# Performance work log

Measured on AMD Instinct MI355X. Metric: run time of the kernel, lower is better.

Reference implementation:

```python
import jax, jax.numpy as jnp
import numpy as np

N_CLIN = 38
N_PIX = 36
N_NODES = N_CLIN + N_PIX  # 74
FV = 128
B = 1024
HID = 512
N_OUT = 1


def _base_edges():
    # Faithful to Network.get_edges: self-edges for all nodes, then for each
    # pixel node i, bidirectional edges to every clinical node.
    ids = np.arange(N_NODES)
    parts = [np.stack([ids, ids])]
    c = np.arange(N_CLIN)
    for i in range(N_CLIN, N_NODES):
        ii = np.full(N_CLIN, i)
        parts.append(np.stack([ii, c]))
        parts.append(np.stack([c, ii]))
    return np.concatenate(parts, axis=1)  # (2, 2810)


def setup_inputs() -> dict:
    key = jax.random.key(0)
    ks = jax.random.split(key, 10)
    base = _base_edges()  # (2, E0)
    # Batched edge index: per-sample copy offset by ind*N_NODES (batch-major order,
    # matching the torch.cat loop).
    offs = np.arange(B)[None, :, None] * N_NODES  # (1, B, 1)
    edge_index = (base[:, None, :] + offs).reshape(2, -1)  # (2, B*E0)
    s = 1.0 / np.sqrt(FV)
    return {
        "clinical_embeddings": jax.random.normal(ks[0], (B, N_CLIN, FV), jnp.float32),
        "image_embeddings": jax.random.normal(ks[1], (B, N_PIX, FV), jnp.float32),
        # RMRM graph-net params (single message-passing layer, fv_dim -> fv_dim)
        "W_self": jax.random.normal(ks[2], (FV, FV), jnp.float32) * s,
        "W_msg": jax.random.normal(ks[3], (FV, FV), jnp.float32) * s,
        "b_g": jnp.zeros((FV,), jnp.float32),
        # OutputBlock MLP params: fv_dim*(n_clinical+1)=4992 -> 512 -> 1
        "W1": jax.random.normal(ks[4], (FV * (N_CLIN + 1), HID), jnp.float32) * (1.0 / np.sqrt(FV * (N_CLIN + 1))),
        "b1": jnp.zeros((HID,), jnp.float32),
        "W2": jax.random.normal(ks[5], (HID, N_OUT), jnp.float32) * (1.0 / np.sqrt(HID)),
        "b2": jnp.zeros((N_OUT,), jnp.float32),
        "edge_index": jnp.asarray(edge_index, jnp.int32),
    }


def reference(clinical_embeddings, image_embeddings, W_self, W_msg, b_g, W1, b1, W2, b2, edge_index):
    # Assemble node features: [B, n_nodes, fv] -> flat [B*n_nodes, fv]
    x = jnp.concatenate([clinical_embeddings, image_embeddings], axis=1)
    x = x.reshape(-1, FV)
    src, dst = edge_index[0], edge_index[1]
    n_total = B * N_NODES
    # Mean-aggregated message passing (RMRM layer): gather + segment-sum
    msg = jax.ops.segment_sum(x[src], dst, num_segments=n_total)  # [B*N, FV]
    deg = jax.ops.segment_sum(jnp.ones_like(src, jnp.float32), dst, num_segments=n_total)
    agg = msg / deg[:, None]
    h = jax.nn.relu(x @ W_self + agg @ W_msg + b_g)  # [B*N, FV]
    h = h.reshape(B, N_NODES, FV)
    graph_fvs_c = h[:, :N_CLIN]          # [B, 38, FV]
    graph_fvs_i = h[:, N_CLIN:]          # [B, 36, FV]
    # AvgPool2d(6,6) over [B, FV, 6, 6] == mean over the 36 pixel nodes
    gap = graph_fvs_i.mean(axis=1)       # [B, FV]
    combined = jnp.concatenate([graph_fvs_c, gap[:, None, :]], axis=1).reshape(B, -1)
    # OutputBlock MLP
    out = jax.nn.relu(combined @ W1 + b1) @ W2 + b2  # [B, 1]
    return out
```

## Files before the change

### kernel.cpp

```cpp
#include <hip/hip_runtime.h>

#define FV 128
#define NCLIN 38
#define NPIX 36
#define NTOT 74
#define BATCH 1024
#define HID 512
#define COMB 4992
#define XPAD 136

typedef __attribute__((ext_vector_type(4))) float f32x4;
typedef __attribute__((ext_vector_type(8))) short s16x8;

#define WS_WCT  0
#define WS_WIT  8192
#define WS_WMT  16384
#define WS_COMB 24576
#define WS_W1T  2580480
#define WS_Z    3858432
#define ZSTRIDE (BATCH * HID)

__device__ __forceinline__ unsigned short bf16_rne(float f) {
    union { float f; unsigned int u; } v; v.f = f;
    unsigned int u = v.u;
    u += 0x7fffu + ((u >> 16) & 1u);
    return (unsigned short)(u >> 16);
}
__device__ __forceinline__ float bf2f(unsigned short h) {
    union { unsigned int u; float f; } v; v.u = ((unsigned int)h) << 16;
    return v.f;
}

__global__ __launch_bounds__(256) void k_static(
    const float* __restrict__ W1, const float* __restrict__ wself,
    const float* __restrict__ wmsg, float* __restrict__ ws)
{
    const int t = threadIdx.x;
    if (blockIdx.x == 78) {
        unsigned short* WcT = (unsigned short*)(ws + WS_WCT);
        unsigned short* WiT = (unsigned short*)(ws + WS_WIT);
        unsigned short* WmT = (unsigned short*)(ws + WS_WMT);
        const int r  = blockIdx.y * 16 + (t >> 4);
        const int f0 = (t & 15) * 8;
#pragma unroll
        for (int j = 0; j < 8; ++j) {
            const int f = f0 + j;
            const int idx = r * 128 + f;
            const float wm = wmsg[idx];
            const float s  = wself[idx];
            WcT[f * 128 + r] = bf16_rne(s + wm * (1.0f / 37.0f));
            WiT[f * 128 + r] = bf16_rne(s + wm * (1.0f / 39.0f));
            WmT[f * 128 + r] = bf16_rne(wm);
        }
        return;
    }
    unsigned short* W1T = (unsigned short*)(ws + WS_W1T);
    const int k0 = blockIdx.x * 64;
    const int n0 = blockIdx.y * 64;
    __shared__ float tile[64][65];
    const int r16 = t >> 4;
    const int c4  = (t & 15) * 4;
#pragma unroll
    for (int p = 0; p < 4; ++p) {
        const int r = p * 16 + r16;
        const float4 v = *(const float4*)&W1[(size_t)(k0 + r) * HID + n0 + c4];
        tile[r][c4 + 0] = v.x; tile[r][c4 + 1] = v.y;
        tile[r][c4 + 2] = v.z; tile[r][c4 + 3] = v.w;
    }
    __syncthreads();
    const int j  = t >> 2;
    const int i0 = (t & 3) * 16;
    unsigned short tmp[16];
#pragma unroll
    for (int s = 0; s < 16; ++s) tmp[s] = bf16_rne(tile[i0 + s][j]);
    unsigned short* dst = &W1T[(size_t)(n0 + j) * COMB + k0 + i0];
    *(uint4*)&dst[0] = *(uint4*)&tmp[0];
    *(uint4*)&dst[8] = *(uint4*)&tmp[8];
}

__global__ __launch_bounds__(256) void k_batch(
    const float* __restrict__ clin, const float* __restrict__ img,
    const float* __restrict__ bg, float* __restrict__ ws)
{
    const int b = blockIdx.x;
    const int t = threadIdx.x;

    __shared__ __align__(16) unsigned short xl[NTOT * XPAD];
    __shared__ __align__(16) unsigned short sab[2 * 128];
    __shared__ float tcv[128];
    __shared__ float tiv[128];

    const float* xc = clin + (size_t)b * NCLIN * FV;
    const float* xi = img  + (size_t)b * NPIX * FV;
    for (int i = t; i < NCLIN * 32; i += 256) {
        const int row = i >> 5, c4 = (i & 31) * 4;
        const float4 v = *(const float4*)&xc[row * 128 + c4];
        ushort4 u;
        u.x = bf16_rne(v.x); u.y = bf16_rne(v.y);
        u.z = bf16_rne(v.z); u.w = bf16_rne(v.w);
        *(ushort4*)&xl[row * XPAD + c4] = u;
    }
    for (int i = t; i < NPIX * 32; i += 256) {
        const int row = i >> 5, c4 = (i & 31) * 4;
        const float4 v = *(const float4*)&xi[row * 128 + c4];
        ushort4 u;
        u.x = bf16_rne(v.x); u.y = bf16_rne(v.y);
        u.z = bf16_rne(v.z); u.w = bf16_rne(v.w);
        *(ushort4*)&xl[(NCLIN + row) * XPAD + c4] = u;
    }
    __syncthreads();

    const int f = t & 127;
    if (t < 128) {
        float s = 0.f;
#pragma unroll
        for (int n = 0; n < NCLIN; ++n) s += bf2f(xl[n * XPAD + f]);
        sab[128 + f] = bf16_rne(s * (1.0f / 39.0f));
    } else {
        float s = 0.f;
#pragma unroll
        for (int n = 0; n < NPIX; ++n) s += bf2f(xl[(NCLIN + n) * XPAD + f]);
        sab[f] = bf16_rne(s * (1.0f / 37.0f));
    }
    __syncthreads();

    const int wave = t >> 6;
    const int lane = t & 63;
    const int l16  = lane & 15;
    const int q    = lane >> 4;
    const int n0   = wave * 32 + l16;

    {
        const unsigned short* WmT = (const unsigned short*)(ws + WS_WMT);
        const int am = (l16 < 2) ? l16 : 0;
        f32x4 ta = {}, tb = {};
#pragma unroll
        for (int kk = 0; kk < 4; ++kk) {
            const int ko = kk * 32 + q * 8;
            const s16x8 av  = *(const s16x8*)&sab[am * 128 + ko];
            const s16x8 bv0 = *(const s16x8*)&WmT[(n0)      * 128 + ko];
            const s16x8 bv1 = *(const s16x8*)&WmT[(n0 + 16) * 128 + ko];
            ta = __builtin_amdgcn_mfma_f32_16x16x32_bf16(av, bv0, ta, 0, 0, 0);
            tb = __builtin_amdgcn_mfma_f32_16x16x32_bf16(av, bv1, tb, 0, 0, 0);
        }
        if (q == 0) {
            const int c0 = wave * 32 + l16;
            const int c1 = c0 + 16;
            const float bg0 = bg[c0], bg1 = bg[c1];
            tcv[c0] = ta[0] + bg0;  tiv[c0] = ta[1] + bg0;
            tcv[c1] = tb[0] + bg1;  tiv[c1] = tb[1] + bg1;
        }
    }
    __syncthreads();

    const unsigned short* WcT = (const unsigned short*)(ws + WS_WCT);
    const unsigned short* WiT = (const unsigned short*)(ws + WS_WIT);
    unsigned short* combined =
        (unsigned short*)(ws + WS_COMB) + (size_t)b * COMB;

#pragma unroll
    for (int phase = 0; phase < 2; ++phase) {
        const int NN   = phase ? NPIX : NCLIN;
        const int xoff = phase ? NCLIN : 0;
        const unsigned short* WT = phase ? WiT : WcT;
        const float* tvv = phase ? tiv : tcv;

        const int r0 = xoff + ((l16      < NN) ? l16      : (NN - 1));
        const int r1 = xoff + ((16 + l16 < NN) ? 16 + l16 : (NN - 1));
        const int r2 = xoff + ((32 + l16 < NN) ? 32 + l16 : (NN - 1));

        f32x4 acc[3][2] = {};
#pragma unroll
        for (int kk = 0; kk < 4; ++kk) {
            const int ko = kk * 32 + q * 8;
            const s16x8 a0 = *(const s16x8*)&xl[r0 * XPAD + ko];
            const s16x8 a1 = *(const s16x8*)&xl[r1 * XPAD + ko];
            const s16x8 a2 = *(const s16x8*)&xl[r2 * XPAD + ko];
            const s16x8 b0 = *(const s16x8*)&WT[(n0)      * 128 + ko];
            const s16x8 b1 = *(const s16x8*)&WT[(n0 + 16) * 128 + ko];
            acc[0][0] = __builtin_amdgcn_mfma_f32_16x16x32_bf16(a0, b0, acc[0][0], 0, 0, 0);
            acc[0][1] = __builtin_amdgcn_mfma_f32_16x16x32_bf16(a0, b1, acc[0][1], 0, 0, 0);
            acc[1][0] = __builtin_amdgcn_mfma_f32_16x16x32_bf16(a1, b0, acc[1][0], 0, 0, 0);
            acc[1][1] = __builtin_amdgcn_mfma_f32_16x16x32_bf16(a1, b1, acc[1][1], 0, 0, 0);
            acc[2][0] = __builtin_amdgcn_mfma_f32_16x16x32_bf16(a2, b0, acc[2][0], 0, 0, 0);
            acc[2][1] = __builtin_amdgcn_mfma_f32_16x16x32_bf16(a2, b1, acc[2][1], 0, 0, 0);
        }

        const float t0 = tvv[wave * 32 + l16];
        const float t1 = tvv[wave * 32 + 16 + l16];

        if (phase == 0) {
#pragma unroll
            for (int rt = 0; rt < 3; ++rt) {
#pragma unroll
                for (int r = 0; r < 4; ++r) {
                    const int node = rt * 16 + q * 4 + r;
                    if (node < NCLIN) {
                        combined[node * 128 + wave * 32 + l16] =
                            bf16_rne(fmaxf(acc[rt][0][r] + t0, 0.f));
                        combined[node * 128 + wave * 32 + 16 + l16] =
                            bf16_rne(fmaxf(acc[rt][1][r] + t1, 0.f));
                    }
                }
            }
        } else {
            float g0 = 0.f, g1 = 0.f;
#pragma unroll
            for (int rt = 0; rt < 3; ++rt) {
#pragma unroll
                for (int r = 0; r < 4; ++r) {
                    const int node = rt * 16 + q * 4 + r;
                    if (node < NPIX) {
                        g0 += fmaxf(acc[rt][0][r] + t0, 0.f);
                        g1 += fmaxf(acc[rt][1][r] + t1, 0.f);
                    }
                }
            }
            g0 += __shfl_xor(g0, 16); g0 += __shfl_xor(g0, 32);
            g1 += __shfl_xor(g1, 16); g1 += __shfl_xor(g1, 32);
            if (q == 0) {
                combined[NCLIN * 128 + wave * 32 + l16] =
                    bf16_rne(g0 * (1.0f / 36.0f));
                combined[NCLIN * 128 + wave * 32 + 16 + l16] =
                    bf16_rne(g1 * (1.0f / 36.0f));
            }
        }
    }
}

__global__ __launch_bounds__(256) void k_gemm_mfma(float* __restrict__ ws)
{
    const unsigned short* Abase = (const unsigned short*)(ws + WS_COMB);
    const unsigned short* Bbase = (const unsigned short*)(ws + WS_W1T);
    const int m0    = blockIdx.x * 128;
    const int n0    = blockIdx.y * 128;
    const int ks    = blockIdx.z;
    const int kbase = (ks < 4) ? 640 * ks : 2560 + 608 * (ks - 4);
    const int kit   = (ks < 4) ? 20 : 19;
    float* Z = ws + WS_Z + (size_t)ks * ZSTRIDE;

    __shared__ __align__(16) unsigned short As[2][128 * 32];
    __shared__ __align__(16) unsigned short Bs[2][128 * 32];

    const int t    = threadIdx.x;
    const int wave = t >> 6;
    const int lane = t & 63;
    const int wm   = (wave & 1) * 64;
    const int wn   = (wave >> 1) * 64;
    const int l16  = lane & 15;
    const int q    = lane >> 4;

    const int srow = t >> 1;
    const int qb   = (t & 1) * 2;
    const unsigned short* gA = Abase + (size_t)(m0 + srow) * COMB + kbase + qb * 8;
    const unsigned short* gB = Bbase + (size_t)(n0 + srow) * COMB + kbase + qb * 8;
    const int sw0 = srow * 32 + ((qb     + (srow >> 1)) & 3) * 8;
    const int sw1 = srow * 32 + ((qb + 1 + (srow >> 1)) & 3) * 8;

    int aoff[4], boff[4];
#pragma unroll
    for (int i = 0; i < 4; ++i) {
        const int Ra = wm + i * 16 + l16;
        aoff[i] = Ra * 32 + ((q + (Ra >> 1)) & 3) * 8;
        const int Rb = wn + i * 16 + l16;
        boff[i] = Rb * 32 + ((q + (Rb >> 1)) & 3) * 8;
    }

    f32x4 acc[4][4] = {};

    *(uint4*)&As[0][sw0] = *(const uint4*)(gA);
    *(uint4*)&As[0][sw1] = *(const uint4*)(gA + 8);
    *(uint4*)&Bs[0][sw0] = *(const uint4*)(gB);
    *(uint4*)&Bs[0][sw1] = *(const uint4*)(gB + 8);

    int cur = 0;
    for (int it = 0; it < kit; ++it) {
        __syncthreads();
        if (it + 1 < kit) {
            const int kk  = (it + 1) * 32;
            const int nxt = cur ^ 1;
            *(uint4*)&As[nxt][sw0] = *(const uint4*)(gA + kk);
            *(uint4*)&As[nxt][sw1] = *(const uint4*)(gA + kk + 8);
            *(uint4*)&Bs[nxt][sw0] = *(const uint4*)(gB + kk);
            *(uint4*)&Bs[nxt][sw1] = *(const uint4*)(gB + kk + 8);
        }

        s16x8 af[4], bf[4];
#pragma unroll
        for (int i = 0; i < 4; ++i) af[i] = *(const s16x8*)&As[cur][aoff[i]];
#pragma unroll
        for (int i = 0; i < 4; ++i) bf[i] = *(const s16x8*)&Bs[cur][boff[i]];

#pragma unroll
        for (int i = 0; i < 4; ++i) {
#pragma unroll
            for (int j = 0; j < 4; ++j) {
                acc[i][j] = __builtin_amdgcn_mfma_f32_16x16x32_bf16(
                    af[i], bf[j], acc[i][j], 0, 0, 0);
            }
        }

        cur ^= 1;
    }

#pragma unroll
    for (int i = 0; i < 4; ++i) {
#pragma unroll
        for (int r = 0; r < 4; ++r) {
            const int mr = m0 + wm + 16 * i + q * 4 + r;
            float* zr = Z + (size_t)mr * HID + n0 + wn + l16;
#pragma unroll
            for (int j = 0; j < 4; ++j) {
                zr[16 * j] = acc[i][j][r];
            }
        }
    }
}

__global__ __launch_bounds__(256) void k_out(
    const float* __restrict__ b1, const float* __restrict__ W2,
    const float* __restrict__ b2, const float* __restrict__ ws,
    float* __restrict__ out)
{
    const int b = blockIdx.x * 4 + (threadIdx.x >> 6);
    const int l = threadIdx.x & 63;
    const float* z = ws + WS_Z + (size_t)b * HID;
    float s = 0.f;
#pragma unroll
    for (int j = 0; j < 8; ++j) {
        const int h = l + j * 64;
        float acc = b1[h];
#pragma unroll
        for (int p = 0; p < 8; ++p) acc += z[(size_t)p * ZSTRIDE + h];
        acc = fmaxf(acc, 0.f);
        s += acc * W2[h];
    }
#pragma unroll
    for (int off = 32; off > 0; off >>= 1) s += __shfl_down(s, off);
    if (l == 0) out[b] = s + b2[0];
}

extern "C" void kernel_launch(void* const* d_in, const int* in_sizes, int n_in,
                              void* d_out, int out_size, void* d_ws, size_t ws_size,
                              hipStream_t stream) {
    const float* clin  = (const float*)d_in[0];
    const float* img   = (const float*)d_in[1];
    const float* wself = (const float*)d_in[2];
    const float* wmsg  = (const float*)d_in[3];
    const float* bg    = (const float*)d_in[4];
    const float* W1    = (const float*)d_in[5];
    const float* b1    = (const float*)d_in[6];
    const float* W2    = (const float*)d_in[7];
    const float* b2    = (const float*)d_in[8];
    float* ws  = (float*)d_ws;
    float* out = (float*)d_out;

    k_static<<<dim3(79, 8), 256, 0, stream>>>(W1, wself, wmsg, ws);
    k_batch <<<dim3(BATCH), 256, 0, stream>>>(clin, img, bg, ws);
    k_gemm_mfma<<<dim3(8, 4, 8), 256, 0, stream>>>(ws);
    k_out<<<dim3(BATCH / 4), 256, 0, stream>>>(b1, W2, b2, ws, out);
}
```

Measured before the change: 150.8 us.

## Fuse four kernels into one persistent kernel with grid-wide atomic barriers

Merges the static weight-conversion, per-batch graph layer, split-K GEMM and output reduction kernels into a single persistent kernel of 256 blocks. The stages are separated by software grid barriers built on agent-scope atomics, and a tiny init kernel resets the barrier counters. This removes launch gaps and tail effects between kernels. In exchange, each block now loops over four batches serially. The W1 transpose is spread over fewer blocks, and the barriers rely on all 256 blocks being co-resident.

```diff
diff --git a/kernel.cpp b/kernel.cpp
--- a/kernel.cpp
+++ b/kernel.cpp
@@ -8,6 +8,7 @@
 #define HID 512
 #define COMB 4992
 #define XPAD 136
+#define NBLK 256
 
 typedef __attribute__((ext_vector_type(4))) float f32x4;
 typedef __attribute__((ext_vector_type(8))) short s16x8;
@@ -18,6 +19,7 @@
 #define WS_COMB 24576
 #define WS_W1T  2580480
 #define WS_Z    3858432
+#define WS_BAR  8052736
 #define ZSTRIDE (BATCH * HID)
 
 __device__ __forceinline__ unsigned short bf16_rne(float f) {
@@ -31,16 +33,63 @@
     return v.f;
 }
 
-__global__ __launch_bounds__(256) void k_static(
-    const float* __restrict__ W1, const float* __restrict__ wself,
-    const float* __restrict__ wmsg, float* __restrict__ ws)
+__device__ __forceinline__ void gbar(int* bar, int idx) {
+    __syncthreads();
+    if (threadIdx.x == 0) {
+        __threadfence();
+        int old = __hip_atomic_fetch_add(&bar[idx * 2], 1,
+                                         __ATOMIC_ACQ_REL, __HIP_MEMORY_SCOPE_AGENT);
+        if (old == NBLK - 1) {
+            __hip_atomic_store(&bar[idx * 2 + 1], 1,
+                               __ATOMIC_RELEASE, __HIP_MEMORY_SCOPE_AGENT);
+        } else {
+            while (!__hip_atomic_load(&bar[idx * 2 + 1],
+                                      __ATOMIC_ACQUIRE, __HIP_MEMORY_SCOPE_AGENT)) {
+                __builtin_amdgcn_s_sleep(1);
+            }
+        }
+    }
+    __syncthreads();
+}
+
+__global__ void k_init(float* __restrict__ ws) {
+    int* bar = (int*)(ws + WS_BAR);
+    if (threadIdx.x < 16) bar[threadIdx.x] = 0;
+}
+
+union __align__(16) Smem {
+    float tile[64][65];
+    struct {
+        unsigned short xl[NTOT * XPAD];
+        unsigned short sab[2 * 128];
+        float tcv[128];
+        float tiv[128];
+    } b;
+    struct {
+        unsigned short As[2][4096];
+        unsigned short Bs[2][4096];
+    } c;
+};
+
+__global__ __launch_bounds__(256) void k_fused(
+    const float* __restrict__ clin, const float* __restrict__ img,
+    const float* __restrict__ wself, const float* __restrict__ wmsg,
+    const float* __restrict__ bg, const float* __restrict__ W1,
+    const float* __restrict__ b1, const float* __restrict__ W2,
+    const float* __restrict__ b2, float* __restrict__ ws,
+    float* __restrict__ out)
 {
-    const int t = threadIdx.x;
-    if (blockIdx.x == 78) {
+    const int blk = blockIdx.x;
+    const int t   = threadIdx.x;
+    int* bar = (int*)(ws + WS_BAR);
+
+    __shared__ Smem sm;
+
+    if (blk < 8) {
         unsigned short* WcT = (unsigned short*)(ws + WS_WCT);
         unsigned short* WiT = (unsigned short*)(ws + WS_WIT);
         unsigned short* WmT = (unsigned short*)(ws + WS_WMT);
-        const int r  = blockIdx.y * 16 + (t >> 4);
+        const int r  = blk * 16 + (t >> 4);
         const int f0 = (t & 15) * 8;
 #pragma unroll
         for (int j = 0; j < 8; ++j) {
@@ -52,292 +101,283 @@
             WiT[f * 128 + r] = bf16_rne(s + wm * (1.0f / 39.0f));
             WmT[f * 128 + r] = bf16_rne(wm);
         }
-        return;
-    }
-    unsigned short* W1T = (unsigned short*)(ws + WS_W1T);
-    const int k0 = blockIdx.x * 64;
-    const int n0 = blockIdx.y * 64;
-    __shared__ float tile[64][65];
-    const int r16 = t >> 4;
-    const int c4  = (t & 15) * 4;
-#pragma unroll
-    for (int p = 0; p < 4; ++p) {
-        const int r = p * 16 + r16;
-        const float4 v = *(const float4*)&W1[(size_t)(k0 + r) * HID + n0 + c4];
-        tile[r][c4 + 0] = v.x; tile[r][c4 + 1] = v.y;
-        tile[r][c4 + 2] = v.z; tile[r][c4 + 3] = v.w;
-    }
-    __syncthreads();
-    const int j  = t >> 2;
-    const int i0 = (t & 3) * 16;
-    unsigned short tmp[16];
-#pragma unroll
-    for (int s = 0; s < 16; ++s) tmp[s] = bf16_rne(tile[i0 + s][j]);
-    unsigned short* dst = &W1T[(size_t)(n0 + j) * COMB + k0 + i0];
-    *(uint4*)&dst[0] = *(uint4*)&tmp[0];
-    *(uint4*)&dst[8] = *(uint4*)&tmp[8];
-}
-
-__global__ __launch_bounds__(256) void k_batch(
-    const float* __restrict__ clin, const float* __restrict__ img,
-    const float* __restrict__ bg, float* __restrict__ ws)
-{
-    const int b = blockIdx.x;
-    const int t = threadIdx.x;
-
-    __shared__ __align__(16) unsigned short xl[NTOT * XPAD];
-    __shared__ __align__(16) unsigned short sab[2 * 128];
-    __shared__ float tcv[128];
-    __shared__ float tiv[128];
-
-    const float* xc = clin + (size_t)b * NCLIN * FV;
-    const float* xi = img  + (size_t)b * NPIX * FV;
-    for (int i = t; i < NCLIN * 32; i += 256) {
-        const int row = i >> 5, c4 = (i & 31) * 4;
-        const float4 v = *(const float4*)&xc[row * 128 + c4];
-        ushort4 u;
-        u.x = bf16_rne(v.x); u.y = bf16_rne(v.y);
-        u.z = bf16_rne(v.z); u.w = bf16_rne(v.w);
-        *(ushort4*)&xl[row * XPAD + c4] = u;
-    }
-    for (int i = t; i < NPIX * 32; i += 256) {
-        const int row = i >> 5, c4 = (i & 31) * 4;
-        const float4 v = *(const float4*)&xi[row * 128 + c4];
-        ushort4 u;
-        u.x = bf16_rne(v.x); u.y = bf16_rne(v.y);
-        u.z = bf16_rne(v.z); u.w = bf16_rne(v.w);
-        *(ushort4*)&xl[(NCLIN + row) * XPAD + c4] = u;
-    }
-    __syncthreads();
-
-    const int f = t & 127;
-    if (t < 128) {
+    }
+    gbar(bar, 0);
+
+    {
+        unsigned short* W1T = (unsigned short*)(ws + WS_W1T);
+        for (int u = blk; u < 624; u += NBLK) {
+            const int k0 = (u >> 3) * 64;
+            const int n0 = (u & 7) * 64;
+            const int r16 = t >> 4;
+            const int c4  = (t & 15) * 4;
+#pragma unroll
+            for (int p = 0; p < 4; ++p) {
+                const int r = p * 16 + r16;
+                const float4 v = *(const float4*)&W1[(size_t)(k0 + r) * HID + n0 + c4];
+                sm.tile[r][c4 + 0] = v.x; sm.tile[r][c4 + 1] = v.y;
+                sm.tile[r][c4 + 2] = v.z; sm.tile[r][c4 + 3] = v.w;
+            }
+            __syncthreads();
+            const int j  = t >> 2;
+            const int i0 = (t & 3) * 16;
+            unsigned short tmp[16];
+#pragma unroll
+            for (int s = 0; s < 16; ++s) tmp[s] = bf16_rne(sm.tile[i0 + s][j]);
+            unsigned short* dst = &W1T[(size_t)(n0 + j) * COMB + k0 + i0];
+            *(uint4*)&dst[0] = *(uint4*)&tmp[0];
+            *(uint4*)&dst[8] = *(uint4*)&tmp[8];
+            __syncthreads();
+        }
+    }
+
+    {
+        const unsigned short* WcT = (const unsigned short*)(ws + WS_WCT);
+        const unsigned short* WiT = (const unsigned short*)(ws + WS_WIT);
+        const unsigned short* WmT = (const unsigned short*)(ws + WS_WMT);
+        const int wave = t >> 6;
+        const int lane = t & 63;
+        const int l16  = lane & 15;
+        const int q    = lane >> 4;
+        const int n0   = wave * 32 + l16;
+
+        for (int bi = 0; bi < 4; ++bi) {
+            const int b = blk + NBLK * bi;
+
+            const float* xc = clin + (size_t)b * NCLIN * FV;
+            const float* xi = img  + (size_t)b * NPIX * FV;
+            for (int i = t; i < NCLIN * 32; i += 256) {
+                const int row = i >> 5, c4 = (i & 31) * 4;
+                const float4 v = *(const float4*)&xc[row * 128 + c4];
+                ushort4 u;
+                u.x = bf16_rne(v.x); u.y = bf16_rne(v.y);
+                u.z = bf16_rne(v.z); u.w = bf16_rne(v.w);
+                *(ushort4*)&sm.b.xl[row * XPAD + c4] = u;
+            }
+            for (int i = t; i < NPIX * 32; i += 256) {
+                const int row = i >> 5, c4 = (i & 31) * 4;
+                const float4 v = *(const float4*)&xi[row * 128 + c4];
+                ushort4 u;
+                u.x = bf16_rne(v.x); u.y = bf16_rne(v.y);
+                u.z = bf16_rne(v.z); u.w = bf16_rne(v.w);
+                *(ushort4*)&sm.b.xl[(NCLIN + row) * XPAD + c4] = u;
+            }
+            __syncthreads();
+
+            const int f = t & 127;
+            if (t < 128) {
+                float s = 0.f;
+#pragma unroll
+                for (int n = 0; n < NCLIN; ++n) s += bf2f(sm.b.xl[n * XPAD + f]);
+                sm.b.sab[128 + f] = bf16_rne(s * (1.0f / 39.0f));
+            } else {
+                float s = 0.f;
+#pragma unroll
+                for (int n = 0; n < NPIX; ++n) s += bf2f(sm.b.xl[(NCLIN + n) * XPAD + f]);
+                sm.b.sab[f] = bf16_rne(s * (1.0f / 37.0f));
+            }
+            __syncthreads();
+
+            {
+                const int am = (l16 < 2) ? l16 : 0;
+                f32x4 ta = {}, tb = {};
+#pragma unroll
+                for (int kk = 0; kk < 4; ++kk) {
+                    const int ko = kk * 32 + q * 8;
+                    const s16x8 av  = *(const s16x8*)&sm.b.sab[am * 128 + ko];
+                    const s16x8 bv0 = *(const s16x8*)&WmT[(n0)      * 128 + ko];
+                    const s16x8 bv1 = *(const s16x8*)&WmT[(n0 + 16) * 128 + ko];
+                    ta = __builtin_amdgcn_mfma_f32_16x16x32_bf16(av, bv0, ta, 0, 0, 0);
+                    tb = __builtin_amdgcn_mfma_f32_16x16x32_bf16(av, bv1, tb, 0, 0, 0);
+                }
+                if (q == 0) {
+                    const int c0 = wave * 32 + l16;
+                    const int c1 = c0 + 16;
+                    const float bg0 = bg[c0], bg1 = bg[c1];
+                    sm.b.tcv[c0] = ta[0] + bg0;  sm.b.tiv[c0] = ta[1] + bg0;
+                    sm.b.tcv[c1] = tb[0] + bg1;  sm.b.tiv[c1] = tb[1] + bg1;
+                }
+            }
+            __syncthreads();
+
+            unsigned short* combined =
+                (unsigned short*)(ws + WS_COMB) + (size_t)b * COMB;
+
+#pragma unroll
+            for (int phase = 0; phase < 2; ++phase) {
+                const int NN   = phase ? NPIX : NCLIN;
+                const int xoff = phase ? NCLIN : 0;
+                const unsigned short* WT = phase ? WiT : WcT;
+                const float* tvv = phase ? sm.b.tiv : sm.b.tcv;
+
+                const int r0 = xoff + ((l16      < NN) ? l16      : (NN - 1));
+                const int r1 = xoff + ((16 + l16 < NN) ? 16 + l16 : (NN - 1));
+                const int r2 = xoff + ((32 + l16 < NN) ? 32 + l16 : (NN - 1));
+
+                f32x4 acc[3][2] = {};
+#pragma unroll
+                for (int kk = 0; kk < 4; ++kk) {
+                    const int ko = kk * 32 + q * 8;
+                    const s16x8 a0 = *(const s16x8*)&sm.b.xl[r0 * XPAD + ko];
+                    const s16x8 a1 = *(const s16x8*)&sm.b.xl[r1 * XPAD + ko];
+                    const s16x8 a2 = *(const s16x8*)&sm.b.xl[r2 * XPAD + ko];
+                    const s16x8 b0 = *(const s16x8*)&WT[(n0)      * 128 + ko];
+                    const s16x8 b1v = *(const s16x8*)&WT[(n0 + 16) * 128 + ko];
+                    acc[0][0] = __builtin_amdgcn_mfma_f32_16x16x32_bf16(a0, b0,  acc[0][0], 0, 0, 0);
+                    acc[0][1] = __builtin_amdgcn_mfma_f32_16x16x32_bf16(a0, b1v, acc[0][1], 0, 0, 0);
+                    acc[1][0] = __builtin_amdgcn_mfma_f32_16x16x32_bf16(a1, b0,  acc[1][0], 0, 0, 0);
+                    acc[1][1] = __builtin_amdgcn_mfma_f32_16x16x32_bf16(a1, b1v, acc[1][1], 0, 0, 0);
+                    acc[2][0] = __builtin_amdgcn_mfma_f32_16x16x32_bf16(a2, b0,  acc[2][0], 0, 0, 0);
+                    acc[2][1] = __builtin_amdgcn_mfma_f32_16x16x32_bf16(a2, b1v, acc[2][1], 0, 0, 0);
+                }
+
+                const float t0 = tvv[wave * 32 + l16];
+                const float t1 = tvv[wave * 32 + 16 + l16];
+
+                if (phase == 0) {
+#pragma unroll
+                    for (int rt = 0; rt < 3; ++rt) {
+#pragma unroll
+                        for (int r = 0; r < 4; ++r) {
+                            const int node = rt * 16 + q * 4 + r;
+                            if (node < NCLIN) {
+                                combined[node * 128 + wave * 32 + l16] =
+                                    bf16_rne(fmaxf(acc[rt][0][r] + t0, 0.f));
+                                combined[node * 128 + wave * 32 + 16 + l16] =
+                                    bf16_rne(fmaxf(acc[rt][1][r] + t1, 0.f));
+                            }
+                        }
+                    }
+                } else {
+                    float g0 = 0.f, g1 = 0.f;
+#pragma unroll
+                    for (int rt = 0; rt < 3; ++rt) {
+#pragma unroll
+                        for (int r = 0; r < 4; ++r) {
+                            const int node = rt * 16 + q * 4 + r;
+                            if (node < NPIX) {
+                                g0 += fmaxf(acc[rt][0][r] + t0, 0.f);
+                                g1 += fmaxf(acc[rt][1][r] + t1, 0.f);
+                            }
+                        }
+                    }
+                    g0 += __shfl_xor(g0, 16); g0 += __shfl_xor(g0, 32);
+                    g1 += __shfl_xor(g1, 16); g1 += __shfl_xor(g1, 32);
+                    if (q == 0) {
+                        combined[NCLIN * 128 + wave * 32 + l16] =
+                            bf16_rne(g0 * (1.0f / 36.0f));
+                        combined[NCLIN * 128 + wave * 32 + 16 + l16] =
+                            bf16_rne(g1 * (1.0f / 36.0f));
+                    }
+                }
+            }
+            __syncthreads();
+        }
+    }
+    gbar(bar, 1);
+
+    {
+        const unsigned short* Abase = (const unsigned short*)(ws + WS_COMB);
+        const unsigned short* Bbase = (const unsigned short*)(ws + WS_W1T);
+        const int m0    = (blk & 7) * 128;
+        const int n0    = ((blk >> 3) & 3) * 128;
+        const int ks    = blk >> 5;
+        const int kbase = (ks < 4) ? 640 * ks : 2560 + 608 * (ks - 4);
+        const int kit   = (ks < 4) ? 20 : 19;
+        float* Z = ws + WS_Z + (size_t)ks * ZSTRIDE;
+
+        const int wave = t >> 6;
+        const int lane = t & 63;
+        const int wm   = (wave & 1) * 64;
+        const int wn   = (wave >> 1) * 64;
+        const int l16  = lane & 15;
+        const int q    = lane >> 4;
+
+        const int srow = t >> 1;
+        const int qb   = (t & 1) * 2;
+        const unsigned short* gA = Abase + (size_t)(m0 + srow) * COMB + kbase + qb * 8;
+        const unsigned short* gB = Bbase + (size_t)(n0 + srow) * COMB + kbase + qb * 8;
+        const int sw0 = srow * 32 + ((qb     + (srow >> 1)) & 3) * 8;
+        const int sw1 = srow * 32 + ((qb + 1 + (srow >> 1)) & 3) * 8;
+
+        int aoff[4], boff[4];
+#pragma unroll
+        for (int i = 0; i < 4; ++i) {
+            const int Ra = wm + i * 16 + l16;
+            aoff[i] = Ra * 32 + ((q + (Ra >> 1)) & 3) * 8;
+            const int Rb = wn + i * 16 + l16;
+            boff[i] = Rb * 32 + ((q + (Rb >> 1)) & 3) * 8;
+        }
+
+        f32x4 acc[4][4] = {};
+
+        *(uint4*)&sm.c.As[0][sw0] = *(const uint4*)(gA);
+        *(uint4*)&sm.c.As[0][sw1] = *(const uint4*)(gA + 8);
+        *(uint4*)&sm.c.Bs[0][sw0] = *(const uint4*)(gB);
+        *(uint4*)&sm.c.Bs[0][sw1] = *(const uint4*)(gB + 8);
+
+        int cur = 0;
+        for (int it = 0; it < kit; ++it) {
+            __syncthreads();
+            if (it + 1 < kit) {
+                const int kk  = (it + 1) * 32;
+                const int nxt = cur ^ 1;
+                *(uint4*)&sm.c.As[nxt][sw0] = *(const uint4*)(gA + kk);
+                *(uint4*)&sm.c.As[nxt][sw1] = *(const uint4*)(gA + kk + 8);
+                *(uint4*)&sm.c.Bs[nxt][sw0] = *(const uint4*)(gB + kk);
+                *(uint4*)&sm.c.Bs[nxt][sw1] = *(const uint4*)(gB + kk + 8);
+            }
+
+            s16x8 af[4], bfr[4];
+#pragma unroll
+            for (int i = 0; i < 4; ++i) af[i]  = *(const s16x8*)&sm.c.As[cur][aoff[i]];
+#pragma unroll
+            for (int i = 0; i < 4; ++i) bfr[i] = *(const s16x8*)&sm.c.Bs[cur][boff[i]];
+
+#pragma unroll
+            for (int i = 0; i < 4; ++i) {
+#pragma unroll
+                for (int j = 0; j < 4; ++j) {
+                    acc[i][j] = __builtin_amdgcn_mfma_f32_16x16x32_bf16(
+                        af[i], bfr[j], acc[i][j], 0, 0, 0);
+                }
+            }
+            cur ^= 1;
+        }
+
+#pragma unroll
+        for (int i = 0; i < 4; ++i) {
+#pragma unroll
+            for (int r = 0; r < 4; ++r) {
+                const int mr = m0 + wm + 16 * i + q * 4 + r;
+                float* zr = Z + (size_t)mr * HID + n0 + wn + l16;
+#pragma unroll
+                for (int j = 0; j < 4; ++j) {
+                    zr[16 * j] = acc[i][j][r];
+                }
+            }
+        }
+    }
+    gbar(bar, 2);
+
+    {
+        const int b = blk * 4 + (t >> 6);
+        const int l = t & 63;
+        const float* z = ws + WS_Z + (size_t)b * HID;
         float s = 0.f;
 #pragma unroll
-        for (int n = 0; n < NCLIN; ++n) s += bf2f(xl[n * XPAD + f]);
-        sab[128 + f] = bf16_rne(s * (1.0f / 39.0f));
-    } else {
-        float s = 0.f;
-#pragma unroll
-        for (int n = 0; n < NPIX; ++n) s += bf2f(xl[(NCLIN + n) * XPAD + f]);
-        sab[f] = bf16_rne(s * (1.0f / 37.0f));
-    }
-    __syncthreads();
-
-    const int wave = t >> 6;
-    const int lane = t & 63;
-    const int l16  = lane & 15;
-    const int q    = lane >> 4;
-    const int n0   = wave * 32 + l16;
-
-    {
-        const unsigned short* WmT = (const unsigned short*)(ws + WS_WMT);
-        const int am = (l16 < 2) ? l16 : 0;
-        f32x4 ta = {}, tb = {};
-#pragma unroll
-        for (int kk = 0; kk < 4; ++kk) {
-            const int ko = kk * 32 + q * 8;
-            const s16x8 av  = *(const s16x8*)&sab[am * 128 + ko];
-            const s16x8 bv0 = *(const s16x8*)&WmT[(n0)      * 128 + ko];
-            const s16x8 bv1 = *(const s16x8*)&WmT[(n0 + 16) * 128 + ko];
-            ta = __builtin_amdgcn_mfma_f32_16x16x32_bf16(av, bv0, ta, 0, 0, 0);
-            tb = __builtin_amdgcn_mfma_f32_16x16x32_bf16(av, bv1, tb, 0, 0, 0);
-        }
-        if (q == 0) {
-            const int c0 = wave * 32 + l16;
-            const int c1 = c0 + 16;
-            const float bg0 = bg[c0], bg1 = bg[c1];
-            tcv[c0] = ta[0] + bg0;  tiv[c0] = ta[1] + bg0;
-            tcv[c1] = tb[0] + bg1;  tiv[c1] = tb[1] + bg1;
-        }
-    }
-    __syncthreads();
-
-    const unsigned short* WcT = (const unsigned short*)(ws + WS_WCT);
-    const unsigned short* WiT = (const unsigned short*)(ws + WS_WIT);
-    unsigned short* combined =
-        (unsigned short*)(ws + WS_COMB) + (size_t)b * COMB;
-
-#pragma unroll
-    for (int phase = 0; phase < 2; ++phase) {
-        const int NN   = phase ? NPIX : NCLIN;
-        const int xoff = phase ? NCLIN : 0;
-        const unsigned short* WT = phase ? WiT : WcT;
-        const float* tvv = phase ? tiv : tcv;
-
-        const int r0 = xoff + ((l16      < NN) ? l16      : (NN - 1));
-        const int r1 = xoff + ((16 + l16 < NN) ? 16 + l16 : (NN - 1));
-        const int r2 = xoff + ((32 + l16 < NN) ? 32 + l16 : (NN - 1));
-
-        f32x4 acc[3][2] = {};
-#pragma unroll
-        for (int kk = 0; kk < 4; ++kk) {
-            const int ko = kk * 32 + q * 8;
-            const s16x8 a0 = *(const s16x8*)&xl[r0 * XPAD + ko];
-            const s16x8 a1 = *(const s16x8*)&xl[r1 * XPAD + ko];
-            const s16x8 a2 = *(const s16x8*)&xl[r2 * XPAD + ko];
-            const s16x8 b0 = *(const s16x8*)&WT[(n0)      * 128 + ko];
-            const s16x8 b1 = *(const s16x8*)&WT[(n0 + 16) * 128 + ko];
-            acc[0][0] = __builtin_amdgcn_mfma_f32_16x16x32_bf16(a0, b0, acc[0][0], 0, 0, 0);
-            acc[0][1] = __builtin_amdgcn_mfma_f32_16x16x32_bf16(a0, b1, acc[0][1], 0, 0, 0);
-            acc[1][0] = __builtin_amdgcn_mfma_f32_16x16x32_bf16(a1, b0, acc[1][0], 0, 0, 0);
-            acc[1][1] = __builtin_amdgcn_mfma_f32_16x16x32_bf16(a1, b1, acc[1][1], 0, 0, 0);
-            acc[2][0] = __builtin_amdgcn_mfma_f32_16x16x32_bf16(a2, b0, acc[2][0], 0, 0, 0);
-            acc[2][1] = __builtin_amdgcn_mfma_f32_16x16x32_bf16(a2, b1, acc[2][1], 0, 0, 0);
-        }
-
-        const float t0 = tvv[wave * 32 + l16];
-        const float t1 = tvv[wave * 32 + 16 + l16];
-
-        if (phase == 0) {
-#pragma unroll
-            for (int rt = 0; rt < 3; ++rt) {
-#pragma unroll
-                for (int r = 0; r < 4; ++r) {
-                    const int node = rt * 16 + q * 4 + r;
-                    if (node < NCLIN) {
-                        combined[node * 128 + wave * 32 + l16] =
-                            bf16_rne(fmaxf(acc[rt][0][r] + t0, 0.f));
-                        combined[node * 128 + wave * 32 + 16 + l16] =
-                            bf16_rne(fmaxf(acc[rt][1][r] + t1, 0.f));
-                    }
-                }
-            }
-        } else {
-            float g0 = 0.f, g1 = 0.f;
-#pragma unroll
-            for (int rt = 0; rt < 3; ++rt) {
-#pragma unroll
-                for (int r = 0; r < 4; ++r) {
-                    const int node = rt * 16 + q * 4 + r;
-                    if (node < NPIX) {
-                        g0 += fmaxf(acc[rt][0][r] + t0, 0.f);
-                        g1 += fmaxf(acc[rt][1][r] + t1, 0.f);
-                    }
-                }
-            }
-            g0 += __shfl_xor(g0, 16); g0 += __shfl_xor(g0, 32);
-            g1 += __shfl_xor(g1, 16); g1 += __shfl_xor(g1, 32);
-            if (q == 0) {
-                combined[NCLIN * 128 + wave * 32 + l16] =
-                    bf16_rne(g0 * (1.0f / 36.0f));
-                combined[NCLIN * 128 + wave * 32 + 16 + l16] =
-                    bf16_rne(g1 * (1.0f / 36.0f));
-            }
-        }
-    }
-}
-
-__global__ __launch_bounds__(256) void k_gemm_mfma(float* __restrict__ ws)
-{
-    const unsigned short* Abase = (const unsigned short*)(ws + WS_COMB);
-    const unsigned short* Bbase = (const unsigned short*)(ws + WS_W1T);
-    const int m0    = blockIdx.x * 128;
-    const int n0    = blockIdx.y * 128;
-    const int ks    = blockIdx.z;
-    const int kbase = (ks < 4) ? 640 * ks : 2560 + 608 * (ks - 4);
-    const int kit   = (ks < 4) ? 20 : 19;
-    float* Z = ws + WS_Z + (size_t)ks * ZSTRIDE;
-
-    __shared__ __align__(16) unsigned short As[2][128 * 32];
-    __shared__ __align__(16) unsigned short Bs[2][128 * 32];
-
-    const int t    = threadIdx.x;
-    const int wave = t >> 6;
-    const int lane = t & 63;
-    const int wm   = (wave & 1) * 64;
-    const int wn   = (wave >> 1) * 64;
-    const int l16  = lane & 15;
-    const int q    = lane >> 4;
-
-    const int srow = t >> 1;
-    const int qb   = (t & 1) * 2;
-    const unsigned short* gA = Abase + (size_t)(m0 + srow) * COMB + kbase + qb * 8;
-    const unsigned short* gB = Bbase + (size_t)(n0 + srow) * COMB + kbase + qb * 8;
-    const int sw0 = srow * 32 + ((qb     + (srow >> 1)) & 3) * 8;
-    const int sw1 = srow * 32 + ((qb + 1 + (srow >> 1)) & 3) * 8;
-
-    int aoff[4], boff[4];
-#pragma unroll
-    for (int i = 0; i < 4; ++i) {
-        const int Ra = wm + i * 16 + l16;
-        aoff[i] = Ra * 32 + ((q + (Ra >> 1)) & 3) * 8;
-        const int Rb = wn + i * 16 + l16;
-        boff[i] = Rb * 32 + ((q + (Rb >> 1)) & 3) * 8;
-    }
-
-    f32x4 acc[4][4] = {};
-
-    *(uint4*)&As[0][sw0] = *(const uint4*)(gA);
-    *(uint4*)&As[0][sw1] = *(const uint4*)(gA + 8);
-    *(uint4*)&Bs[0][sw0] = *(const uint4*)(gB);
-    *(uint4*)&Bs[0][sw1] = *(const uint4*)(gB + 8);
-
-    int cur = 0;
-    for (int it = 0; it < kit; ++it) {
-        __syncthreads();
-        if (it + 1 < kit) {
-            const int kk  = (it + 1) * 32;
-            const int nxt = cur ^ 1;
-            *(uint4*)&As[nxt][sw0] = *(const uint4*)(gA + kk);
-            *(uint4*)&As[nxt][sw1] = *(const uint4*)(gA + kk + 8);
-            *(uint4*)&Bs[nxt][sw0] = *(const uint4*)(gB + kk);
-            *(uint4*)&Bs[nxt][sw1] = *(const uint4*)(gB + kk + 8);
-        }
-
-        s16x8 af[4], bf[4];
-#pragma unroll
-        for (int i = 0; i < 4; ++i) af[i] = *(const s16x8*)&As[cur][aoff[i]];
-#pragma unroll
-        for (int i = 0; i < 4; ++i) bf[i] = *(const s16x8*)&Bs[cur][boff[i]];
-
-#pragma unroll
-        for (int i = 0; i < 4; ++i) {
-#pragma unroll
-            for (int j = 0; j < 4; ++j) {
-                acc[i][j] = __builtin_amdgcn_mfma_f32_16x16x32_bf16(
-                    af[i], bf[j], acc[i][j], 0, 0, 0);
-            }
-        }
-
-        cur ^= 1;
-    }
-
-#pragma unroll
-    for (int i = 0; i < 4; ++i) {
-#pragma unroll
-        for (int r = 0; r < 4; ++r) {
-            const int mr = m0 + wm + 16 * i + q * 4 + r;
-            float* zr = Z + (size_t)mr * HID + n0 + wn + l16;
-#pragma unroll
-            for (int j = 0; j < 4; ++j) {
-                zr[16 * j] = acc[i][j][r];
-            }
-        }
-    }
-}
-
-__global__ __launch_bounds__(256) void k_out(
-    const float* __restrict__ b1, const float* __restrict__ W2,
-    const float* __restrict__ b2, const float* __restrict__ ws,
-    float* __restrict__ out)
-{
-    const int b = blockIdx.x * 4 + (threadIdx.x >> 6);
-    const int l = threadIdx.x & 63;
-    const float* z = ws + WS_Z + (size_t)b * HID;
-    float s = 0.f;
-#pragma unroll
-    for (int j = 0; j < 8; ++j) {
-        const int h = l + j * 64;
-        float acc = b1[h];
-#pragma unroll
-        for (int p = 0; p < 8; ++p) acc += z[(size_t)p * ZSTRIDE + h];
-        acc = fmaxf(acc, 0.f);
-        s += acc * W2[h];
-    }
-#pragma unroll
-    for (int off = 32; off > 0; off >>= 1) s += __shfl_down(s, off);
-    if (l == 0) out[b] = s + b2[0];
+        for (int j = 0; j < 8; ++j) {
+            const int h = l + j * 64;
+            float acc = b1[h];
+#pragma unroll
+            for (int p = 0; p < 8; ++p) acc += z[(size_t)p * ZSTRIDE + h];
+            acc = fmaxf(acc, 0.f);
+            s += acc * W2[h];
+        }
+#pragma unroll
+        for (int off = 32; off > 0; off >>= 1) s += __shfl_down(s, off);
+        if (l == 0) out[b] = s + b2[0];
+    }
 }
 
 extern "C" void kernel_launch(void* const* d_in, const int* in_sizes, int n_in,
@@ -355,8 +395,7 @@
     float* ws  = (float*)d_ws;
     float* out = (float*)d_out;
 
-    k_static<<<dim3(79, 8), 256, 0, stream>>>(W1, wself, wmsg, ws);
-    k_batch <<<dim3(BATCH), 256, 0, stream>>>(clin, img, bg, ws);
-    k_gemm_mfma<<<dim3(8, 4, 8), 256, 0, stream>>>(ws);
-    k_out<<<dim3(BATCH / 4), 256, 0, stream>>>(b1, W2, b2, ws, out);
-}
+    k_init<<<dim3(1), 64, 0, stream>>>(ws);
+    k_fused<<<dim3(NBLK), 256, 0, stream>>>(clin, img, wself, wmsg, bg,
+                                            W1, b1, W2, b2, ws, out);
+}
```

After: 276.9 us. 1.84x slower.
